# Performance work log

Measured on AMD Instinct MI355X. Metric: run time of the kernel, lower is better.

## Reference

```python
import jax, jax.numpy as jnp
import numpy as np

D_STATE = 16


def setup_inputs() -> dict:
    key = jax.random.key(0)
    ks = jax.random.split(key, 7)
    B, S, D = 8, 4096, 64
    ds = D_STATE
    x = jax.random.normal(ks[0], (B, S, D), dtype=jnp.float32)
    # Selection layers modeled as Linear(d_model, out). W_A scaled small so the
    # random transition matrices are contractive over 4096 steps.
    W_A = jax.random.normal(ks[1], (D, ds * ds), dtype=jnp.float32) * 0.01
    b_A = jnp.zeros((ds * ds,), dtype=jnp.float32)
    W_B = jax.random.normal(ks[2], (D, ds * D), dtype=jnp.float32) * 0.05
    b_B = jnp.zeros((ds * D,), dtype=jnp.float32)
    W_C = jax.random.normal(ks[3], (D, ds * D), dtype=jnp.float32) * 0.05
    b_C = jnp.zeros((ds * D,), dtype=jnp.float32)
    return {"x": x, "W_A": W_A, "b_A": b_A, "W_B": W_B, "b_B": b_B,
            "W_C": W_C, "b_C": b_C}


def reference(x, W_A, b_A, W_B, b_B, W_C, b_C):
    B, S, D = x.shape
    ds = D_STATE
    # Input-dependent (selective) parameters per timestep
    A = (x @ W_A + b_A).reshape(B, S, ds, ds)      # [B,S,ds,ds]
    Bm = (x @ W_B + b_B).reshape(B, S, ds, D)      # [B,S,ds,D]
    Cm = (x @ W_C + b_C).reshape(B, S, ds, D)      # [B,S,ds,D]
    # Pre-contract B_t @ x_t once: [B,S,ds]
    Bx = jnp.einsum('bsnd,bsd->bsn', Bm, x)

    def step(h, inputs):
        A_t, Bx_t = inputs                          # [B,ds,ds], [B,ds]
        h = jnp.einsum('bij,bj->bi', A_t, h) + Bx_t
        return h, h

    h0 = jnp.zeros((B, ds), dtype=x.dtype)
    _, hs = jax.lax.scan(step, h0,
                         (jnp.swapaxes(A, 0, 1), jnp.swapaxes(Bx, 0, 1)))
    hs = jnp.swapaxes(hs, 0, 1)                     # [B,S,ds]
    # output_t = C_t^T @ h_t  -> [B,S,D]
    return jnp.einsum('bsnd,bsn->bsd', Cm, hs)
```

## Files before the change

kernel.cpp:

```cpp
#include <hip/hip_runtime.h>

#define BATCH   8
#define SEQ     4096
#define DM      64
#define DS      16
#define BS      (BATCH*SEQ)
#define CHUNK   32
#define NCH     (SEQ/CHUNK)
#define NCH_TOT (BATCH*NCH)

typedef __attribute__((ext_vector_type(8))) __bf16 bf16x8;
typedef __attribute__((ext_vector_type(4))) float  f32x4;

__device__ __forceinline__ unsigned short f2bf(float f) {
  unsigned int u = __float_as_uint(f);
  u += 0x7fffu + ((u >> 16) & 1u);
  return (unsigned short)(u >> 16);
}
__device__ __forceinline__ float bflo(unsigned int u) { return __uint_as_float(u << 16); }
__device__ __forceinline__ float bfhi(unsigned int u) { return __uint_as_float(u & 0xffff0000u); }

#define AS_I 20
#define AS_T 324

__global__ __launch_bounds__(256) void k0_cast(
    const float* __restrict__ x, const float* __restrict__ WA,
    const float* __restrict__ WB, const float* __restrict__ WC,
    unsigned short* __restrict__ xb, unsigned short* __restrict__ WAt,
    unsigned short* __restrict__ WBt, unsigned short* __restrict__ WCt)
{
  const int b = blockIdx.x;
  if (b < 1024) {
    const int i = (b * 256 + threadIdx.x) * 8;
    float4 v0 = *(const float4*)(x + i);
    float4 v1 = *(const float4*)(x + i + 4);
    ushort4 o0 = {f2bf(v0.x), f2bf(v0.y), f2bf(v0.z), f2bf(v0.w)};
    ushort4 o1 = {f2bf(v1.x), f2bf(v1.y), f2bf(v1.z), f2bf(v1.w)};
    *(ushort4*)(xb + i)     = o0;
    *(ushort4*)(xb + i + 4) = o1;
  } else {
    const int o = (b - 1024) * 256 + threadIdx.x;
    if (o < 16384) {
      const int c = o >> 6, e = o & 63;
      WAt[o] = f2bf(WA[e * 256 + c]);
    } else if (o < 16384 + 65536) {
      const int p = o - 16384;
      const int c = p >> 6, e = p & 63;
      WBt[p] = f2bf(WB[e * 1024 + c]);
    } else {
      const int p = o - 16384 - 65536;
      const int c = p >> 6, e = p & 63;
      WCt[p] = f2bf(WC[e * 1024 + c]);
    }
  }
}

__global__ __launch_bounds__(256) void g_B(
    const unsigned short* __restrict__ xb, const unsigned short* __restrict__ WBt,
    const float* __restrict__ bB, const float* __restrict__ x,
    float* __restrict__ Bx_ws)
{
  __shared__ float xs[64][68];
  __shared__ float bBs[1024];
  const int tid  = threadIdx.x;
  const int lane = tid & 63;
  const int l15  = lane & 15;
  const int quad = lane >> 4;
  const int w    = tid >> 6;
  const int t0   = blockIdx.x * 64;
  const int tw   = t0 + w * 16;

  {
    const float4* xg = (const float4*)(x + (size_t)t0 * DM);
    #pragma unroll
    for (int i = 0; i < 4; ++i) {
      const int f4 = tid + 256 * i;
      ((float4*)&xs[f4 >> 4][0])[f4 & 15] = xg[f4];
    }
    ((float4*)bBs)[tid] = ((const float4*)bB)[tid];
  }

  const bf16x8* xv = (const bf16x8*)(xb + (size_t)(tw + l15) * 64);
  bf16x8 a0 = xv[quad];
  bf16x8 a1 = xv[quad + 4];
  __syncthreads();

  #pragma unroll 2
  for (int n = 0; n < 16; ++n) {
    f32x4 ac[4];
    #pragma unroll
    for (int r = 0; r < 4; ++r) {
      const bf16x8* wv = (const bf16x8*)(WBt + (size_t)((n * 4 + r) * 16 + l15) * 64);
      f32x4 t = {0.f, 0.f, 0.f, 0.f};
      t = __builtin_amdgcn_mfma_f32_16x16x32_bf16(a0, wv[quad],     t, 0, 0, 0);
      t = __builtin_amdgcn_mfma_f32_16x16x32_bf16(a1, wv[quad + 4], t, 0, 0, 0);
      ac[r] = t;
    }
    float part[4] = {0.f, 0.f, 0.f, 0.f};
    #pragma unroll
    for (int r = 0; r < 4; ++r) {
      const float bb = bBs[n * 64 + r * 16 + l15];
      #pragma unroll
      for (int reg = 0; reg < 4; ++reg) {
        const int tl = w * 16 + quad * 4 + reg;
        part[reg] = fmaf(ac[r][reg] + bb, xs[tl][r * 16 + l15], part[reg]);
      }
    }
    #pragma unroll
    for (int off = 1; off < 16; off <<= 1) {
      #pragma unroll
      for (int reg = 0; reg < 4; ++reg)
        part[reg] += __shfl_xor(part[reg], off, 64);
    }
    if (l15 == 0) {
      #pragma unroll
      for (int reg = 0; reg < 4; ++reg)
        Bx_ws[(size_t)(tw + quad * 4 + reg) * DS + n] = part[reg];
    }
  }
}

__global__ __launch_bounds__(256) void gk2(
    const unsigned short* __restrict__ xb, const unsigned short* __restrict__ WAt,
    const float* __restrict__ bA, const float* __restrict__ Bx_ws,
    unsigned short* __restrict__ Wt_ws, float* __restrict__ u_ws,
    float* __restrict__ P_ws, float* __restrict__ v_ws)
{
  __shared__ unsigned short As[64 * AS_T];
  __shared__ __align__(16) float bxs[64][16];
  __shared__ __align__(16) float us[2][16];
  const int tid  = threadIdx.x;
  const int lane = tid & 63;
  const int l15  = lane & 15;
  const int quad = lane >> 4;
  const int w    = tid >> 6;
  const int t0   = blockIdx.x * 64;
  const int tw   = w * 16;

  ((float4*)&bxs[0][0])[tid] = ((const float4*)(Bx_ws + (size_t)t0 * DS))[tid];
  if (tid < 32) us[tid >> 4][tid & 15] = 0.f;

  {
    const bf16x8* xv = (const bf16x8*)(xb + (size_t)(t0 + tw + l15) * 64);
    bf16x8 a0 = xv[quad];
    bf16x8 a1 = xv[quad + 4];
    #pragma unroll 2
    for (int ns = 0; ns < 16; ++ns) {
      const bf16x8* wv = (const bf16x8*)(WAt + (size_t)(ns * 16 + l15) * 64);
      f32x4 acc = {0.f, 0.f, 0.f, 0.f};
      acc = __builtin_amdgcn_mfma_f32_16x16x32_bf16(a0, wv[quad],     acc, 0, 0, 0);
      acc = __builtin_amdgcn_mfma_f32_16x16x32_bf16(a1, wv[quad + 4], acc, 0, 0, 0);
      const float bias = bA[ns * 16 + l15];
      #pragma unroll
      for (int r = 0; r < 4; ++r)
        As[(tw + quad * 4 + r) * AS_T + ns * AS_I + l15] = f2bf(acc[r] + bias);
    }
  }
  __syncthreads();

  if (w < 2) {
    const int tb = w * 32;
    bf16x8 wb;
    #pragma unroll
    for (int j = 0; j < 8; ++j) wb[j] = (__bf16)((quad * 8 + j == l15) ? 1.f : 0.f);
    f32x4 d = {0.f, 0.f, 0.f, 0.f};
    const int qq = quad & 1;

    #pragma unroll 1
    for (int t = 0; t < CHUNK; ++t) {
      const int tl = tb + t;
      const unsigned short* rp = &As[tl * AS_T + l15 * AS_I];
      uint2 r0 = *(const uint2*)(rp);
      uint2 r1 = *(const uint2*)(rp + 4);
      uint2 r2 = *(const uint2*)(rp + 8);
      uint2 r3 = *(const uint2*)(rp + 12);

      uint4 abits;
      if (quad == 0)      abits = make_uint4(r0.x, r0.y, r1.x, r1.y);
      else if (quad == 1) abits = make_uint4(r2.x, r2.y, r3.x, r3.y);
      else                abits = make_uint4(0u, 0u, 0u, 0u);
      bf16x8 af = *(bf16x8*)&abits;

      f32x4 z4 = {0.f, 0.f, 0.f, 0.f};
      d = __builtin_amdgcn_mfma_f32_16x16x32_bf16(af, wb, z4, 0, 0, 0);

      float nu = bxs[tl][l15];
      {
        float4 U0 = *(const float4*)&us[w][0];
        float4 U1 = *(const float4*)&us[w][4];
        float4 U2 = *(const float4*)&us[w][8];
        float4 U3 = *(const float4*)&us[w][12];
        nu = fmaf(bflo(r0.x), U0.x, nu); nu = fmaf(bfhi(r0.x), U0.y, nu);
        nu = fmaf(bflo(r0.y), U0.z, nu); nu = fmaf(bfhi(r0.y), U0.w, nu);
        nu = fmaf(bflo(r1.x), U1.x, nu); nu = fmaf(bfhi(r1.x), U1.y, nu);
        nu = fmaf(bflo(r1.y), U1.z, nu); nu = fmaf(bfhi(r1.y), U1.w, nu);
        nu = fmaf(bflo(r2.x), U2.x, nu); nu = fmaf(bfhi(r2.x), U2.y, nu);
        nu = fmaf(bflo(r2.y), U2.z, nu); nu = fmaf(bfhi(r2.y), U2.w, nu);
        nu = fmaf(bflo(r3.x), U3.x, nu); nu = fmaf(bfhi(r3.x), U3.y, nu);
        nu = fmaf(bflo(r3.y), U3.z, nu); nu = fmaf(bfhi(r3.y), U3.w, nu);
      }

      bf16x8 nb;
      nb[0] = (__bf16)__shfl(d[0], (2 * qq + 0) * 16 + l15, 64);
      nb[1] = (__bf16)__shfl(d[1], (2 * qq + 0) * 16 + l15, 64);
      nb[2] = (__bf16)__shfl(d[2], (2 * qq + 0) * 16 + l15, 64);
      nb[3] = (__bf16)__shfl(d[3], (2 * qq + 0) * 16 + l15, 64);
      nb[4] = (__bf16)__shfl(d[0], (2 * qq + 1) * 16 + l15, 64);
      nb[5] = (__bf16)__shfl(d[1], (2 * qq + 1) * 16 + l15, 64);
      nb[6] = (__bf16)__shfl(d[2], (2 * qq + 1) * 16 + l15, 64);
      nb[7] = (__bf16)__shfl(d[3], (2 * qq + 1) * 16 + l15, 64);
      wb = nb;

      if (quad == 0) {
        us[w][l15] = nu;
        u_ws[(size_t)(t0 + tl) * DS + l15] = nu;
      }
      #pragma unroll
      for (int r = 0; r < 4; ++r)
        As[tl * AS_T + (quad * 4 + r) * AS_I + l15] = f2bf(d[r]);
    }

    const int chunk = blockIdx.x * 2 + w;
    #pragma unroll
    for (int r = 0; r < 4; ++r)
      P_ws[(size_t)chunk * 256 + (quad * 4 + r) * 16 + l15] = d[r];
    if (quad == 0) v_ws[(size_t)chunk * DS + l15] = us[w][l15];
  }
  __syncthreads();

  {
    uint4* Wg = (uint4*)(Wt_ws + (size_t)t0 * 256);
    #pragma unroll 1
    for (int z = 0; z < 8; ++z) {
      const int p4 = z * 256 + tid;
      const int f  = p4 * 8;
      const int t  = f >> 8, i = (f >> 4) & 15, k = f & 15;
      const unsigned short* sp = &As[t * AS_T + i * AS_I + k];
      uint2 lo = *(const uint2*)(sp);
      uint2 hi = *(const uint2*)(sp + 4);
      Wg[p4] = make_uint4(lo.x, lo.y, hi.x, hi.y);
    }
  }
}

__global__ __launch_bounds__(128) void k3_boundary(
    const float* __restrict__ P_ws, const float* __restrict__ v_ws,
    float* __restrict__ hb_ws)
{
  const int tid = threadIdx.x;
  const int b = tid >> 4;
  const int r = tid & 15;
  float h = 0.f;

  const float4* Pr = (const float4*)&P_ws[(size_t)(b * NCH) * 256 + r * 16];
  float4 c0 = Pr[0], c1 = Pr[1], c2 = Pr[2], c3 = Pr[3];
  float vc = v_ws[(size_t)(b * NCH) * DS + r];

  for (int c = 0; c < NCH; ++c) {
    const int chunk = b * NCH + c;
    float4 n0 = c0, n1 = c1, n2 = c2, n3 = c3; float nv = 0.f;
    if (c < NCH - 1) {
      const float4* Pn = (const float4*)&P_ws[(size_t)(chunk + 1) * 256 + r * 16];
      n0 = Pn[0]; n1 = Pn[1]; n2 = Pn[2]; n3 = Pn[3];
      nv = v_ws[(size_t)(chunk + 1) * DS + r];
    }
    hb_ws[(size_t)chunk * DS + r] = h;
    float acc = vc;
    acc += c0.x*__shfl(h, 0,16) + c0.y*__shfl(h, 1,16) + c0.z*__shfl(h, 2,16) + c0.w*__shfl(h, 3,16);
    acc += c1.x*__shfl(h, 4,16) + c1.y*__shfl(h, 5,16) + c1.z*__shfl(h, 6,16) + c1.w*__shfl(h, 7,16);
    acc += c2.x*__shfl(h, 8,16) + c2.y*__shfl(h, 9,16) + c2.z*__shfl(h,10,16) + c2.w*__shfl(h,11,16);
    acc += c3.x*__shfl(h,12,16) + c3.y*__shfl(h,13,16) + c3.z*__shfl(h,14,16) + c3.w*__shfl(h,15,16);
    h = acc;
    c0 = n0; c1 = n1; c2 = n2; c3 = n3; vc = nv;
  }
}

__global__ __launch_bounds__(256) void k4n(
    const unsigned short* __restrict__ Wt_ws, const float* __restrict__ u_ws,
    const float* __restrict__ hb_ws, float* __restrict__ hs_ws)
{
  const int g = blockIdx.x * 256 + threadIdx.x;
  const int t = g >> 4, i = g & 15;
  const int chunk = t >> 5;
  const uint4* wr = (const uint4*)(Wt_ws + (size_t)t * 256 + i * 16);
  uint4 wa = wr[0], wbv = wr[1];
  const float4* hp = (const float4*)(hb_ws + (size_t)chunk * DS);
  float4 h0 = hp[0], h1 = hp[1], h2 = hp[2], h3 = hp[3];
  float acc = u_ws[(size_t)t * DS + i];
  acc = fmaf(bflo(wa.x),  h0.x, acc); acc = fmaf(bfhi(wa.x),  h0.y, acc);
  acc = fmaf(bflo(wa.y),  h0.z, acc); acc = fmaf(bfhi(wa.y),  h0.w, acc);
  acc = fmaf(bflo(wa.z),  h1.x, acc); acc = fmaf(bfhi(wa.z),  h1.y, acc);
  acc = fmaf(bflo(wa.w),  h1.z, acc); acc = fmaf(bfhi(wa.w),  h1.w, acc);
  acc = fmaf(bflo(wbv.x), h2.x, acc); acc = fmaf(bfhi(wbv.x), h2.y, acc);
  acc = fmaf(bflo(wbv.y), h2.z, acc); acc = fmaf(bfhi(wbv.y), h2.w, acc);
  acc = fmaf(bflo(wbv.z), h3.x, acc); acc = fmaf(bfhi(wbv.z), h3.y, acc);
  acc = fmaf(bflo(wbv.w), h3.z, acc); acc = fmaf(bfhi(wbv.w), h3.w, acc);
  hs_ws[(size_t)t * DS + i] = acc;
}

__global__ __launch_bounds__(256) void g_C(
    const unsigned short* __restrict__ xb, const unsigned short* __restrict__ WCt,
    const float* __restrict__ bC, const float* __restrict__ hs_ws,
    float* __restrict__ out)
{
  __shared__ float hsh[64][17];
  __shared__ float bCs[1024];
  const int tid  = threadIdx.x;
  const int lane = tid & 63;
  const int l15  = lane & 15;
  const int quad = lane >> 4;
  const int w    = tid >> 6;
  const int t0   = blockIdx.x * 64;
  const int tw   = t0 + w * 16;

  {
    float4 hv = ((const float4*)(hs_ws + (size_t)t0 * DS))[tid];
    const int t = tid >> 2, n0 = (tid & 3) * 4;
    hsh[t][n0] = hv.x; hsh[t][n0+1] = hv.y; hsh[t][n0+2] = hv.z; hsh[t][n0+3] = hv.w;
    ((float4*)bCs)[tid] = ((const float4*)bC)[tid];
  }

  const bf16x8* xv = (const bf16x8*)(xb + (size_t)(tw + l15) * 64);
  bf16x8 a0 = xv[quad];
  bf16x8 a1 = xv[quad + 4];
  __syncthreads();

  f32x4 ota[4];
  #pragma unroll
  for (int r = 0; r < 4; ++r) ota[r] = (f32x4){0.f, 0.f, 0.f, 0.f};

  #pragma unroll 2
  for (int n = 0; n < 16; ++n) {
    f32x4 ac[4];
    #pragma unroll
    for (int r = 0; r < 4; ++r) {
      const bf16x8* wv = (const bf16x8*)(WCt + (size_t)((n * 4 + r) * 16 + l15) * 64);
      f32x4 t = {0.f, 0.f, 0.f, 0.f};
      t = __builtin_amdgcn_mfma_f32_16x16x32_bf16(a0, wv[quad],     t, 0, 0, 0);
      t = __builtin_amdgcn_mfma_f32_16x16x32_bf16(a1, wv[quad + 4], t, 0, 0, 0);
      ac[r] = t;
    }
    float hn[4];
    #pragma unroll
    for (int reg = 0; reg < 4; ++reg) hn[reg] = hsh[w * 16 + quad * 4 + reg][n];
    #pragma unroll
    for (int r = 0; r < 4; ++r) {
      const float bc = bCs[n * 64 + r * 16 + l15];
      #pragma unroll
      for (int reg = 0; reg < 4; ++reg)
        ota[r][reg] = fmaf(ac[r][reg] + bc, hn[reg], ota[r][reg]);
    }
  }

  #pragma unroll
  for (int r = 0; r < 4; ++r)
    #pragma unroll
    for (int reg = 0; reg < 4; ++reg)
      out[(size_t)(tw + quad * 4 + reg) * DM + r * 16 + l15] = ota[r][reg];
}

extern "C" void kernel_launch(void* const* d_in, const int* in_sizes, int n_in,
                              void* d_out, int out_size, void* d_ws, size_t ws_size,
                              hipStream_t stream) {
  const float* x  = (const float*)d_in[0];
  const float* WA = (const float*)d_in[1];
  const float* bA = (const float*)d_in[2];
  const float* WB = (const float*)d_in[3];
  const float* bB = (const float*)d_in[4];
  const float* WC = (const float*)d_in[5];
  const float* bC = (const float*)d_in[6];
  float* out = (float*)d_out;

  float* ws    = (float*)d_ws;
  float* Bx_ws = ws;
  float* P_ws  = Bx_ws + (size_t)BS * DS;
  float* v_ws  = P_ws  + (size_t)NCH_TOT * 256;
  float* hb_ws = v_ws  + (size_t)NCH_TOT * DS;
  float* hs_ws = hb_ws + (size_t)NCH_TOT * DS;
  float* u_ws  = hs_ws + (size_t)BS * DS;
  unsigned short* xb    = (unsigned short*)(u_ws + (size_t)BS * DS);
  unsigned short* WAt   = xb  + (size_t)BS * 64;
  unsigned short* WBt   = WAt + 256 * 64;
  unsigned short* WCt   = WBt + 1024 * 64;
  unsigned short* Wt_ws = WCt + 1024 * 64;

  k0_cast    <<<1600,      256, 0, stream>>>(x, WA, WB, WC, xb, WAt, WBt, WCt);
  g_B        <<<BS / 64,   256, 0, stream>>>(xb, WBt, bB, x, Bx_ws);
  gk2        <<<BS / 64,   256, 0, stream>>>(xb, WAt, bA, Bx_ws, Wt_ws, u_ws, P_ws, v_ws);
  k3_boundary<<<1,         128, 0, stream>>>(P_ws, v_ws, hb_ws);
  k4n        <<<BS * 16 / 256, 256, 0, stream>>>(Wt_ws, u_ws, hb_ws, hs_ws);
  g_C        <<<BS / 64,   256, 0, stream>>>(xb, WCt, bC, hs_ws, out);
}
```

Measured before the change: 212.4 us.

## Fuse B-projection into chunk scan, split boundary scan hierarchically, fuse hidden expansion into C

Merges g_B into the chunk-local scan kernel so Bx stays in shared memory (aliasing smem buffers), and merges the per-timestep hidden state reconstruction (k4n) into the C-projection kernel. The serial single-block boundary scan over 128 chunks per batch is replaced by a three-level scheme: compose chunk transitions into supergroups in parallel, scan 8 supergroups serially, then expand within supergroups in parallel. This removes intermediate global round-trips and shortens the serial critical path, at the cost of extra launches and bf16 rounding of composed transition products. An FMA reorder in the inner loop also appears.

```diff
diff --git a/kernel.cpp b/kernel.cpp
--- a/kernel.cpp
+++ b/kernel.cpp
@@ -8,6 +8,8 @@
 #define CHUNK   32
 #define NCH     (SEQ/CHUNK)
 #define NCH_TOT (BATCH*NCH)
+#define SG      16
+#define NSG     (NCH_TOT/SG)
 
 typedef __attribute__((ext_vector_type(8))) __bf16 bf16x8;
 typedef __attribute__((ext_vector_type(4))) float  f32x4;
@@ -55,20 +57,27 @@
   }
 }
 
-__global__ __launch_bounds__(256) void g_B(
+__global__ __launch_bounds__(256) void g1(
     const unsigned short* __restrict__ xb, const unsigned short* __restrict__ WBt,
     const float* __restrict__ bB, const float* __restrict__ x,
-    float* __restrict__ Bx_ws)
-{
-  __shared__ float xs[64][68];
-  __shared__ float bBs[1024];
+    const unsigned short* __restrict__ WAt, const float* __restrict__ bA,
+    unsigned short* __restrict__ Wt_ws, float* __restrict__ u_ws,
+    float* __restrict__ P_ws, float* __restrict__ v_ws)
+{
+  __shared__ __align__(16) unsigned char smem[64 * AS_T * 2];
+  float (*xs)[68]     = (float (*)[68])smem;
+  float* bBs          = (float*)(smem + 17408);
+  unsigned short* As  = (unsigned short*)smem;
+  __shared__ __align__(16) float bxs[64][16];
+  __shared__ __align__(16) float us[2][16];
+
   const int tid  = threadIdx.x;
   const int lane = tid & 63;
   const int l15  = lane & 15;
   const int quad = lane >> 4;
   const int w    = tid >> 6;
   const int t0   = blockIdx.x * 64;
-  const int tw   = t0 + w * 16;
+  const int twl  = w * 16;
 
   {
     const float4* xg = (const float4*)(x + (size_t)t0 * DM);
@@ -78,9 +87,10 @@
       ((float4*)&xs[f4 >> 4][0])[f4 & 15] = xg[f4];
     }
     ((float4*)bBs)[tid] = ((const float4*)bB)[tid];
-  }
-
-  const bf16x8* xv = (const bf16x8*)(xb + (size_t)(tw + l15) * 64);
+    if (tid < 32) us[tid >> 4][tid & 15] = 0.f;
+  }
+
+  const bf16x8* xv = (const bf16x8*)(xb + (size_t)(t0 + twl + l15) * 64);
   bf16x8 a0 = xv[quad];
   bf16x8 a1 = xv[quad + 4];
   __syncthreads();
@@ -102,7 +112,7 @@
       const float bb = bBs[n * 64 + r * 16 + l15];
       #pragma unroll
       for (int reg = 0; reg < 4; ++reg) {
-        const int tl = w * 16 + quad * 4 + reg;
+        const int tl = twl + quad * 4 + reg;
         part[reg] = fmaf(ac[r][reg] + bb, xs[tl][r * 16 + l15], part[reg]);
       }
     }
@@ -115,46 +125,21 @@
     if (l15 == 0) {
       #pragma unroll
       for (int reg = 0; reg < 4; ++reg)
-        Bx_ws[(size_t)(tw + quad * 4 + reg) * DS + n] = part[reg];
-    }
-  }
-}
-
-__global__ __launch_bounds__(256) void gk2(
-    const unsigned short* __restrict__ xb, const unsigned short* __restrict__ WAt,
-    const float* __restrict__ bA, const float* __restrict__ Bx_ws,
-    unsigned short* __restrict__ Wt_ws, float* __restrict__ u_ws,
-    float* __restrict__ P_ws, float* __restrict__ v_ws)
-{
-  __shared__ unsigned short As[64 * AS_T];
-  __shared__ __align__(16) float bxs[64][16];
-  __shared__ __align__(16) float us[2][16];
-  const int tid  = threadIdx.x;
-  const int lane = tid & 63;
-  const int l15  = lane & 15;
-  const int quad = lane >> 4;
-  const int w    = tid >> 6;
-  const int t0   = blockIdx.x * 64;
-  const int tw   = w * 16;
-
-  ((float4*)&bxs[0][0])[tid] = ((const float4*)(Bx_ws + (size_t)t0 * DS))[tid];
-  if (tid < 32) us[tid >> 4][tid & 15] = 0.f;
-
-  {
-    const bf16x8* xv = (const bf16x8*)(xb + (size_t)(t0 + tw + l15) * 64);
-    bf16x8 a0 = xv[quad];
-    bf16x8 a1 = xv[quad + 4];
-    #pragma unroll 2
-    for (int ns = 0; ns < 16; ++ns) {
-      const bf16x8* wv = (const bf16x8*)(WAt + (size_t)(ns * 16 + l15) * 64);
-      f32x4 acc = {0.f, 0.f, 0.f, 0.f};
-      acc = __builtin_amdgcn_mfma_f32_16x16x32_bf16(a0, wv[quad],     acc, 0, 0, 0);
-      acc = __builtin_amdgcn_mfma_f32_16x16x32_bf16(a1, wv[quad + 4], acc, 0, 0, 0);
-      const float bias = bA[ns * 16 + l15];
-      #pragma unroll
-      for (int r = 0; r < 4; ++r)
-        As[(tw + quad * 4 + r) * AS_T + ns * AS_I + l15] = f2bf(acc[r] + bias);
-    }
+        bxs[twl + quad * 4 + reg][n] = part[reg];
+    }
+  }
+  __syncthreads();
+
+  #pragma unroll 2
+  for (int ns = 0; ns < 16; ++ns) {
+    const bf16x8* wv = (const bf16x8*)(WAt + (size_t)(ns * 16 + l15) * 64);
+    f32x4 acc = {0.f, 0.f, 0.f, 0.f};
+    acc = __builtin_amdgcn_mfma_f32_16x16x32_bf16(a0, wv[quad],     acc, 0, 0, 0);
+    acc = __builtin_amdgcn_mfma_f32_16x16x32_bf16(a1, wv[quad + 4], acc, 0, 0, 0);
+    const float bias = bA[ns * 16 + l15];
+    #pragma unroll
+    for (int r = 0; r < 4; ++r)
+      As[(twl + quad * 4 + r) * AS_T + ns * AS_I + l15] = f2bf(acc[r] + bias);
   }
   __syncthreads();
 
@@ -193,10 +178,10 @@
         nu = fmaf(bflo(r0.x), U0.x, nu); nu = fmaf(bfhi(r0.x), U0.y, nu);
         nu = fmaf(bflo(r0.y), U0.z, nu); nu = fmaf(bfhi(r0.y), U0.w, nu);
         nu = fmaf(bflo(r1.x), U1.x, nu); nu = fmaf(bfhi(r1.x), U1.y, nu);
-        nu = fmaf(bflo(r1.y), U1.z, nu); nu = fmaf(bfhi(r1.y), U1.w, nu);
         nu = fmaf(bflo(r2.x), U2.x, nu); nu = fmaf(bfhi(r2.x), U2.y, nu);
         nu = fmaf(bflo(r2.y), U2.z, nu); nu = fmaf(bfhi(r2.y), U2.w, nu);
         nu = fmaf(bflo(r3.x), U3.x, nu); nu = fmaf(bfhi(r3.x), U3.y, nu);
+        nu = fmaf(bflo(r1.y), U1.z, nu); nu = fmaf(bfhi(r1.y), U1.w, nu);
         nu = fmaf(bflo(r3.y), U3.z, nu); nu = fmaf(bfhi(r3.y), U3.w, nu);
       }
 
@@ -243,27 +228,109 @@
   }
 }
 
-__global__ __launch_bounds__(128) void k3_boundary(
+__global__ __launch_bounds__(256) void k3a(
     const float* __restrict__ P_ws, const float* __restrict__ v_ws,
-    float* __restrict__ hb_ws)
+    float* __restrict__ Q_ws, float* __restrict__ w_ws)
+{
+  __shared__ float wsv[4][16];
+  const int tid  = threadIdx.x;
+  const int lane = tid & 63;
+  const int l15  = lane & 15;
+  const int quad = lane >> 4;
+  const int wv   = tid >> 6;
+  const int s    = blockIdx.x * 4 + wv;
+  const int qq   = quad & 1;
+
+  if (lane < 16) wsv[wv][lane] = 0.f;
+  bf16x8 wb;
+  #pragma unroll
+  for (int j = 0; j < 8; ++j) wb[j] = (__bf16)((quad * 8 + j == l15) ? 1.f : 0.f);
+  f32x4 d = {0.f, 0.f, 0.f, 0.f};
+
+  #pragma unroll 1
+  for (int t = 0; t < SG; ++t) {
+    const int chunk = s * SG + t;
+    float4 p0 = {0.f,0.f,0.f,0.f}, p1 = {0.f,0.f,0.f,0.f};
+    if (quad < 2) {
+      const float4* pr = (const float4*)(P_ws + (size_t)chunk * 256 + l15 * 16 + quad * 8);
+      p0 = pr[0]; p1 = pr[1];
+    }
+    bf16x8 af;
+    af[0] = (__bf16)p0.x; af[1] = (__bf16)p0.y; af[2] = (__bf16)p0.z; af[3] = (__bf16)p0.w;
+    af[4] = (__bf16)p1.x; af[5] = (__bf16)p1.y; af[6] = (__bf16)p1.z; af[7] = (__bf16)p1.w;
+
+    f32x4 z4 = {0.f, 0.f, 0.f, 0.f};
+    d = __builtin_amdgcn_mfma_f32_16x16x32_bf16(af, wb, z4, 0, 0, 0);
+
+    float part = 0.f;
+    if (quad < 2) {
+      const float* wrow = &wsv[wv][quad * 8];
+      part = p0.x*wrow[0] + p0.y*wrow[1] + p0.z*wrow[2] + p0.w*wrow[3]
+           + p1.x*wrow[4] + p1.y*wrow[5] + p1.z*wrow[6] + p1.w*wrow[7];
+    }
+    part += __shfl_xor(part, 16, 64);
+    const float nv = v_ws[(size_t)chunk * DS + l15];
+
+    bf16x8 nb;
+    nb[0] = (__bf16)__shfl(d[0], (2 * qq + 0) * 16 + l15, 64);
+    nb[1] = (__bf16)__shfl(d[1], (2 * qq + 0) * 16 + l15, 64);
+    nb[2] = (__bf16)__shfl(d[2], (2 * qq + 0) * 16 + l15, 64);
+    nb[3] = (__bf16)__shfl(d[3], (2 * qq + 0) * 16 + l15, 64);
+    nb[4] = (__bf16)__shfl(d[0], (2 * qq + 1) * 16 + l15, 64);
+    nb[5] = (__bf16)__shfl(d[1], (2 * qq + 1) * 16 + l15, 64);
+    nb[6] = (__bf16)__shfl(d[2], (2 * qq + 1) * 16 + l15, 64);
+    nb[7] = (__bf16)__shfl(d[3], (2 * qq + 1) * 16 + l15, 64);
+    wb = nb;
+
+    if (quad == 0) wsv[wv][l15] = part + nv;
+  }
+
+  #pragma unroll
+  for (int r = 0; r < 4; ++r)
+    Q_ws[(size_t)s * 256 + (quad * 4 + r) * 16 + l15] = d[r];
+  if (quad == 0) w_ws[(size_t)s * DS + l15] = wsv[wv][l15];
+}
+
+__global__ __launch_bounds__(128) void k3b(
+    const float* __restrict__ Q_ws, const float* __restrict__ w_ws,
+    float* __restrict__ hbg_ws)
 {
   const int tid = threadIdx.x;
   const int b = tid >> 4;
   const int r = tid & 15;
   float h = 0.f;
 
-  const float4* Pr = (const float4*)&P_ws[(size_t)(b * NCH) * 256 + r * 16];
-  float4 c0 = Pr[0], c1 = Pr[1], c2 = Pr[2], c3 = Pr[3];
-  float vc = v_ws[(size_t)(b * NCH) * DS + r];
-
-  for (int c = 0; c < NCH; ++c) {
-    const int chunk = b * NCH + c;
-    float4 n0 = c0, n1 = c1, n2 = c2, n3 = c3; float nv = 0.f;
-    if (c < NCH - 1) {
-      const float4* Pn = (const float4*)&P_ws[(size_t)(chunk + 1) * 256 + r * 16];
-      n0 = Pn[0]; n1 = Pn[1]; n2 = Pn[2]; n3 = Pn[3];
-      nv = v_ws[(size_t)(chunk + 1) * DS + r];
-    }
+  #pragma unroll 1
+  for (int g = 0; g < 8; ++g) {
+    const int s = b * 8 + g;
+    const float4* Pr = (const float4*)&Q_ws[(size_t)s * 256 + r * 16];
+    float4 c0 = Pr[0], c1 = Pr[1], c2 = Pr[2], c3 = Pr[3];
+    const float vc = w_ws[(size_t)s * DS + r];
+    hbg_ws[(size_t)s * DS + r] = h;
+    float acc = vc;
+    acc += c0.x*__shfl(h, 0,16) + c0.y*__shfl(h, 1,16) + c0.z*__shfl(h, 2,16) + c0.w*__shfl(h, 3,16);
+    acc += c1.x*__shfl(h, 4,16) + c1.y*__shfl(h, 5,16) + c1.z*__shfl(h, 6,16) + c1.w*__shfl(h, 7,16);
+    acc += c2.x*__shfl(h, 8,16) + c2.y*__shfl(h, 9,16) + c2.z*__shfl(h,10,16) + c2.w*__shfl(h,11,16);
+    acc += c3.x*__shfl(h,12,16) + c3.y*__shfl(h,13,16) + c3.z*__shfl(h,14,16) + c3.w*__shfl(h,15,16);
+    h = acc;
+  }
+}
+
+__global__ __launch_bounds__(256) void k3c(
+    const float* __restrict__ P_ws, const float* __restrict__ v_ws,
+    const float* __restrict__ hbg_ws, float* __restrict__ hb_ws)
+{
+  const int tid = threadIdx.x;
+  const int s = blockIdx.x * 16 + (tid >> 4);
+  const int r = tid & 15;
+  float h = hbg_ws[(size_t)s * DS + r];
+
+  #pragma unroll 1
+  for (int t = 0; t < SG; ++t) {
+    const int chunk = s * SG + t;
+    const float4* Pr = (const float4*)&P_ws[(size_t)chunk * 256 + r * 16];
+    float4 c0 = Pr[0], c1 = Pr[1], c2 = Pr[2], c3 = Pr[3];
+    const float vc = v_ws[(size_t)chunk * DS + r];
     hb_ws[(size_t)chunk * DS + r] = h;
     float acc = vc;
     acc += c0.x*__shfl(h, 0,16) + c0.y*__shfl(h, 1,16) + c0.z*__shfl(h, 2,16) + c0.w*__shfl(h, 3,16);
@@ -271,36 +338,13 @@
     acc += c2.x*__shfl(h, 8,16) + c2.y*__shfl(h, 9,16) + c2.z*__shfl(h,10,16) + c2.w*__shfl(h,11,16);
     acc += c3.x*__shfl(h,12,16) + c3.y*__shfl(h,13,16) + c3.z*__shfl(h,14,16) + c3.w*__shfl(h,15,16);
     h = acc;
-    c0 = n0; c1 = n1; c2 = n2; c3 = n3; vc = nv;
-  }
-}
-
-__global__ __launch_bounds__(256) void k4n(
-    const unsigned short* __restrict__ Wt_ws, const float* __restrict__ u_ws,
-    const float* __restrict__ hb_ws, float* __restrict__ hs_ws)
-{
-  const int g = blockIdx.x * 256 + threadIdx.x;
-  const int t = g >> 4, i = g & 15;
-  const int chunk = t >> 5;
-  const uint4* wr = (const uint4*)(Wt_ws + (size_t)t * 256 + i * 16);
-  uint4 wa = wr[0], wbv = wr[1];
-  const float4* hp = (const float4*)(hb_ws + (size_t)chunk * DS);
-  float4 h0 = hp[0], h1 = hp[1], h2 = hp[2], h3 = hp[3];
-  float acc = u_ws[(size_t)t * DS + i];
-  acc = fmaf(bflo(wa.x),  h0.x, acc); acc = fmaf(bfhi(wa.x),  h0.y, acc);
-  acc = fmaf(bflo(wa.y),  h0.z, acc); acc = fmaf(bfhi(wa.y),  h0.w, acc);
-  acc = fmaf(bflo(wa.z),  h1.x, acc); acc = fmaf(bfhi(wa.z),  h1.y, acc);
-  acc = fmaf(bflo(wa.w),  h1.z, acc); acc = fmaf(bfhi(wa.w),  h1.w, acc);
-  acc = fmaf(bflo(wbv.x), h2.x, acc); acc = fmaf(bfhi(wbv.x), h2.y, acc);
-  acc = fmaf(bflo(wbv.y), h2.z, acc); acc = fmaf(bfhi(wbv.y), h2.w, acc);
-  acc = fmaf(bflo(wbv.z), h3.x, acc); acc = fmaf(bfhi(wbv.z), h3.y, acc);
-  acc = fmaf(bflo(wbv.w), h3.z, acc); acc = fmaf(bfhi(wbv.w), h3.w, acc);
-  hs_ws[(size_t)t * DS + i] = acc;
-}
-
-__global__ __launch_bounds__(256) void g_C(
+  }
+}
+
+__global__ __launch_bounds__(256) void g2(
     const unsigned short* __restrict__ xb, const unsigned short* __restrict__ WCt,
-    const float* __restrict__ bC, const float* __restrict__ hs_ws,
+    const float* __restrict__ bC, const unsigned short* __restrict__ Wt_ws,
+    const float* __restrict__ u_ws, const float* __restrict__ hb_ws,
     float* __restrict__ out)
 {
   __shared__ float hsh[64][17];
@@ -311,16 +355,32 @@
   const int quad = lane >> 4;
   const int w    = tid >> 6;
   const int t0   = blockIdx.x * 64;
-  const int tw   = t0 + w * 16;
-
-  {
-    float4 hv = ((const float4*)(hs_ws + (size_t)t0 * DS))[tid];
-    const int t = tid >> 2, n0 = (tid & 3) * 4;
-    hsh[t][n0] = hv.x; hsh[t][n0+1] = hv.y; hsh[t][n0+2] = hv.z; hsh[t][n0+3] = hv.w;
-    ((float4*)bCs)[tid] = ((const float4*)bC)[tid];
-  }
-
-  const bf16x8* xv = (const bf16x8*)(xb + (size_t)(tw + l15) * 64);
+  const int twl  = w * 16;
+
+  ((float4*)bCs)[tid] = ((const float4*)bC)[tid];
+
+  #pragma unroll
+  for (int z = 0; z < 4; ++z) {
+    const int gcell = z * 256 + tid;
+    const int tl = gcell >> 4, i = gcell & 15;
+    const int t = t0 + tl;
+    const uint4* wr = (const uint4*)(Wt_ws + (size_t)t * 256 + i * 16);
+    uint4 wa = wr[0], wbv = wr[1];
+    const float4* hp = (const float4*)(hb_ws + (size_t)(t >> 5) * DS);
+    float4 h0 = hp[0], h1 = hp[1], h2 = hp[2], h3 = hp[3];
+    float acc = u_ws[(size_t)t * DS + i];
+    acc = fmaf(bflo(wa.x),  h0.x, acc); acc = fmaf(bfhi(wa.x),  h0.y, acc);
+    acc = fmaf(bflo(wa.y),  h0.z, acc); acc = fmaf(bfhi(wa.y),  h0.w, acc);
+    acc = fmaf(bflo(wa.z),  h1.x, acc); acc = fmaf(bfhi(wa.z),  h1.y, acc);
+    acc = fmaf(bflo(wa.w),  h1.z, acc); acc = fmaf(bfhi(wa.w),  h1.w, acc);
+    acc = fmaf(bflo(wbv.x), h2.x, acc); acc = fmaf(bfhi(wbv.x), h2.y, acc);
+    acc = fmaf(bflo(wbv.y), h2.z, acc); acc = fmaf(bfhi(wbv.y), h2.w, acc);
+    acc = fmaf(bflo(wbv.z), h3.x, acc); acc = fmaf(bfhi(wbv.z), h3.y, acc);
+    acc = fmaf(bflo(wbv.w), h3.z, acc); acc = fmaf(bfhi(wbv.w), h3.w, acc);
+    hsh[tl][i] = acc;
+  }
+
+  const bf16x8* xv = (const bf16x8*)(xb + (size_t)(t0 + twl + l15) * 64);
   bf16x8 a0 = xv[quad];
   bf16x8 a1 = xv[quad + 4];
   __syncthreads();
@@ -342,7 +402,7 @@
     }
     float hn[4];
     #pragma unroll
-    for (int reg = 0; reg < 4; ++reg) hn[reg] = hsh[w * 16 + quad * 4 + reg][n];
+    for (int reg = 0; reg < 4; ++reg) hn[reg] = hsh[twl + quad * 4 + reg][n];
     #pragma unroll
     for (int r = 0; r < 4; ++r) {
       const float bc = bCs[n * 64 + r * 16 + l15];
@@ -356,7 +416,7 @@
   for (int r = 0; r < 4; ++r)
     #pragma unroll
     for (int reg = 0; reg < 4; ++reg)
-      out[(size_t)(tw + quad * 4 + reg) * DM + r * 16 + l15] = ota[r][reg];
+      out[(size_t)(t0 + twl + quad * 4 + reg) * DM + r * 16 + l15] = ota[r][reg];
 }
 
 extern "C" void kernel_launch(void* const* d_in, const int* in_sizes, int n_in,
@@ -371,23 +431,24 @@
   const float* bC = (const float*)d_in[6];
   float* out = (float*)d_out;
 
-  float* ws    = (float*)d_ws;
-  float* Bx_ws = ws;
-  float* P_ws  = Bx_ws + (size_t)BS * DS;
-  float* v_ws  = P_ws  + (size_t)NCH_TOT * 256;
-  float* hb_ws = v_ws  + (size_t)NCH_TOT * DS;
-  float* hs_ws = hb_ws + (size_t)NCH_TOT * DS;
-  float* u_ws  = hs_ws + (size_t)BS * DS;
-  unsigned short* xb    = (unsigned short*)(u_ws + (size_t)BS * DS);
+  float* ws     = (float*)d_ws;
+  float* P_ws   = ws;
+  float* v_ws   = P_ws   + (size_t)NCH_TOT * 256;
+  float* u_ws   = v_ws   + (size_t)NCH_TOT * DS;
+  float* Q_ws   = u_ws   + (size_t)BS * DS;
+  float* w_ws   = Q_ws   + (size_t)NSG * 256;
+  float* hbg_ws = w_ws   + (size_t)NSG * DS;
+  float* hb_ws  = hbg_ws + (size_t)NSG * DS;
+  unsigned short* xb    = (unsigned short*)(hb_ws + (size_t)NCH_TOT * DS);
   unsigned short* WAt   = xb  + (size_t)BS * 64;
   unsigned short* WBt   = WAt + 256 * 64;
   unsigned short* WCt   = WBt + 1024 * 64;
   unsigned short* Wt_ws = WCt + 1024 * 64;
 
-  k0_cast    <<<1600,      256, 0, stream>>>(x, WA, WB, WC, xb, WAt, WBt, WCt);
-  g_B        <<<BS / 64,   256, 0, stream>>>(xb, WBt, bB, x, Bx_ws);
-  gk2        <<<BS / 64,   256, 0, stream>>>(xb, WAt, bA, Bx_ws, Wt_ws, u_ws, P_ws, v_ws);
-  k3_boundary<<<1,         128, 0, stream>>>(P_ws, v_ws, hb_ws);
-  k4n        <<<BS * 16 / 256, 256, 0, stream>>>(Wt_ws, u_ws, hb_ws, hs_ws);
-  g_C        <<<BS / 64,   256, 0, stream>>>(xb, WCt, bC, hs_ws, out);
-}
+  k0_cast <<<1600,    256, 0, stream>>>(x, WA, WB, WC, xb, WAt, WBt, WCt);
+  g1      <<<BS / 64, 256, 0, stream>>>(xb, WBt, bB, x, WAt, bA, Wt_ws, u_ws, P_ws, v_ws);
+  k3a     <<<NSG / 4, 256, 0, stream>>>(P_ws, v_ws, Q_ws, w_ws);
+  k3b     <<<1,       128, 0, stream>>>(Q_ws, w_ws, hbg_ws);
+  k3c     <<<4,       256, 0, stream>>>(P_ws, v_ws, hbg_ws, hb_ws);
+  g2      <<<BS / 64, 256, 0, stream>>>(xb, WCt, bC, Wt_ws, u_ws, hb_ws, out);
+}
```

Result: faster. 185.6 us (-12.6%).
